# Optimization experiments

Hardware: AMD Instinct MI355X
Metric: run time of the kernel (lower is better)

## Reference

```python
import jax, jax.numpy as jnp
import numpy as np

TAU = 0.2
N_CLUSTERS = 8
FOURIER_K = 8
LATENT_DIM = 64
B = 131072
N_MINUTES = 1440
TWO_PI = 2.0 * np.pi


def setup_inputs() -> dict:
    key = jax.random.key(0)
    ks = jax.random.split(key, 6)
    item_static_emb = jax.random.normal(ks[0], (B, LATENT_DIM), dtype=jnp.float32) * 0.1
    thetas = jax.random.uniform(ks[1], (B,), dtype=jnp.float32) * TWO_PI  # absolute time phase in [0, 2pi)
    cluster_prototypes = jax.random.normal(ks[2], (N_CLUSTERS, LATENT_DIM), dtype=jnp.float32) * 0.1
    fourier_a0 = jax.random.normal(ks[3], (N_CLUSTERS, LATENT_DIM), dtype=jnp.float32) * 0.1
    fourier_a = jax.random.normal(ks[4], (N_CLUSTERS, FOURIER_K, LATENT_DIM), dtype=jnp.float32) * 0.1
    fourier_b = jax.random.normal(ks[5], (N_CLUSTERS, FOURIER_K, LATENT_DIM), dtype=jnp.float32) * 0.1
    return {
        "item_static_emb": item_static_emb,
        "thetas": thetas,
        "cluster_prototypes": cluster_prototypes,
        "fourier_a0": fourier_a0,
        "fourier_a": fourier_a,
        "fourier_b": fourier_b,
    }


def reference(item_static_emb, thetas, cluster_prototypes, fourier_a0, fourier_a, fourier_b):
    # Soft cluster routing: (B, n_clusters)
    scores = jnp.matmul(item_static_emb, cluster_prototypes.T) / TAU
    P = jax.nn.softmax(scores, axis=1)

    # Time-indexed minute bucket; torch builds tables from linspace(0, 2pi, 1440)
    # so the angle for bucket m is m * 2pi/1439.
    minute_indices = jnp.clip((thetas / TWO_PI * N_MINUTES).astype(jnp.int32), 0, N_MINUTES - 1)
    k_seq = jnp.arange(1, FOURIER_K + 1, dtype=jnp.float32)  # (K,)
    angles = minute_indices.astype(jnp.float32) * (TWO_PI / (N_MINUTES - 1))  # (B,)
    k_angles = angles[:, None] * k_seq[None, :]  # (B, K)
    cos_vals = jnp.cos(k_angles)  # (B, K)
    sin_vals = jnp.sin(k_angles)  # (B, K)

    # Fourier-series evaluation per cluster: (B, n_clusters, d)
    a_term = jnp.einsum('bk,nkd->bnd', cos_vals, fourier_a)
    b_term = jnp.einsum('bk,nkd->bnd', sin_vals, fourier_b)
    F_theta = fourier_a0[None, :, :] + a_term + b_term  # (B, n_clusters, d)

    # Softmax-weighted mixture combine: (B, d)
    item_dynamic_emb = jnp.einsum('bn,bnd->bd', P, F_theta)
    return item_dynamic_emb, P
```

## Files before the change

kernel.cpp:

```cpp
#include <hip/hip_runtime.h>
#include <hip/hip_fp16.h>
#include <math.h>

#define D 64
#define NC 8
#define FK 8
#define NMIN 1440
#define TWO_PI_F 6.28318530717958647692f

#define TSZ ((size_t)NMIN * NC * D)

__global__ __launch_bounds__(256) void build_table_kernel(
    const float* __restrict__ a0,
    const float* __restrict__ fa,
    const float* __restrict__ fb,
    __half* __restrict__ T)
{
    const int m = blockIdx.x;
    const int t = threadIdx.x;
    const int d  = t & (D - 1);
    const int n0 = t >> 6;
    const float angle = (float)m * (TWO_PI_F / (float)(NMIN - 1));

    float c[FK], s[FK];
    float s1, c1;
    sincosf(angle, &s1, &c1);
    c[0] = c1; s[0] = s1;
    {
        const float tw = 2.0f * c1;
        float cp = 1.0f, sp = 0.0f;
        float cc = c1, ss = s1;
#pragma unroll
        for (int k = 1; k < FK; ++k) {
            const float cn = fmaf(tw, cc, -cp);
            const float sn = fmaf(tw, ss, -sp);
            cp = cc; sp = ss; cc = cn; ss = sn;
            c[k] = cc; s[k] = ss;
        }
    }

#pragma unroll
    for (int j = 0; j < 2; ++j) {
        const int n = n0 + 4 * j;
        float v = a0[n * D + d];
#pragma unroll
        for (int k = 0; k < FK; ++k) {
            v = fmaf(c[k], fa[(n * FK + k) * D + d], v);
            v = fmaf(s[k], fb[(n * FK + k) * D + d], v);
        }
        T[(size_t)(m * NC + n) * D + d] = __float2half(v);
    }
}

__device__ __forceinline__ float grp8_allreduce_sum(float v) {
    int t;
    t = __builtin_amdgcn_update_dpp(0, __float_as_int(v), 0xB1, 0xF, 0xF, true);
    v += __int_as_float(t);
    t = __builtin_amdgcn_update_dpp(0, __float_as_int(v), 0x4E, 0xF, 0xF, true);
    v += __int_as_float(t);
    t = __builtin_amdgcn_update_dpp(0, __float_as_int(v), 0x141, 0xF, 0xF, true);
    v += __int_as_float(t);
    return v;
}

__global__ __launch_bounds__(256) void mix_kernel8(
    const float* __restrict__ emb,
    const float* __restrict__ thetas,
    const float* __restrict__ proto,
    const __half* __restrict__ T,
    float* __restrict__ out_emb,
    float* __restrict__ out_P,
    int B)
{
    __shared__ float4 sproto[NC * (D / 4)];
    if (threadIdx.x < NC * (D / 4)) {
        sproto[threadIdx.x] = ((const float4*)proto)[threadIdx.x];
    }
    __syncthreads();

    const int t = blockIdx.x * 256 + threadIdx.x;
    const int b = t >> 3;
    const int j = t & 7;
    if (b >= B) return;

    const float th = thetas[b];
    int m = (int)((th / TWO_PI_F) * (float)NMIN);
    m = m < 0 ? 0 : (m > NMIN - 1 ? NMIN - 1 : m);

    const float4* __restrict__ e4 = (const float4*)emb + (size_t)b * (D / 4);
    const float4 ev0 = e4[j];
    const float4 ev1 = e4[j + 8];

    const uint2* __restrict__ t2 = (const uint2*)(T + (size_t)m * NC * D);
    uint2 ua[NC], ub[NC];
#pragma unroll
    for (int n = 0; n < NC; ++n) {
        ua[n] = t2[n * 16 + j];
        ub[n] = t2[n * 16 + j + 8];
    }

    float sc[NC];
#pragma unroll
    for (int n = 0; n < NC; ++n) {
        const float4 pa = sproto[n * (D / 4) + j];
        const float4 pb = sproto[n * (D / 4) + j + 8];
        float v = ev0.x * pa.x;
        v = fmaf(ev0.y, pa.y, v);
        v = fmaf(ev0.z, pa.z, v);
        v = fmaf(ev0.w, pa.w, v);
        v = fmaf(ev1.x, pb.x, v);
        v = fmaf(ev1.y, pb.y, v);
        v = fmaf(ev1.z, pb.z, v);
        v = fmaf(ev1.w, pb.w, v);
        sc[n] = v;
    }

#pragma unroll
    for (int n = 0; n < NC; ++n) {
        sc[n] = grp8_allreduce_sum(sc[n]);
    }

    float mx = -1e30f;
#pragma unroll
    for (int n = 0; n < NC; ++n) { sc[n] *= 5.0f; mx = fmaxf(mx, sc[n]); }
    float sum = 0.0f;
#pragma unroll
    for (int n = 0; n < NC; ++n) { sc[n] = __expf(sc[n] - mx); sum += sc[n]; }
    const float inv = 1.0f / sum;
#pragma unroll
    for (int n = 0; n < NC; ++n) sc[n] *= inv;

    float4 acc0 = make_float4(0.f, 0.f, 0.f, 0.f);
    float4 acc1 = make_float4(0.f, 0.f, 0.f, 0.f);
#pragma unroll
    for (int n = 0; n < NC; ++n) {
        const float pw = sc[n];
        const float2 a01 = __half22float2(*(const __half2*)&ua[n].x);
        const float2 a23 = __half22float2(*(const __half2*)&ua[n].y);
        const float2 b01 = __half22float2(*(const __half2*)&ub[n].x);
        const float2 b23 = __half22float2(*(const __half2*)&ub[n].y);
        acc0.x = fmaf(pw, a01.x, acc0.x);
        acc0.y = fmaf(pw, a01.y, acc0.y);
        acc0.z = fmaf(pw, a23.x, acc0.z);
        acc0.w = fmaf(pw, a23.y, acc0.w);
        acc1.x = fmaf(pw, b01.x, acc1.x);
        acc1.y = fmaf(pw, b01.y, acc1.y);
        acc1.z = fmaf(pw, b23.x, acc1.z);
        acc1.w = fmaf(pw, b23.y, acc1.w);
    }

    float4* __restrict__ o4 = (float4*)out_emb + (size_t)b * (D / 4);
    o4[j]     = acc0;
    o4[j + 8] = acc1;

    if (j == 0) {
        ((float4*)out_P)[(size_t)b * 2 + 0] = make_float4(sc[0], sc[1], sc[2], sc[3]);
    } else if (j == 4) {
        ((float4*)out_P)[(size_t)b * 2 + 1] = make_float4(sc[4], sc[5], sc[6], sc[7]);
    }
}

__global__ __launch_bounds__(256) void fused_fallback(
    const float* __restrict__ emb,
    const float* __restrict__ thetas,
    const float* __restrict__ proto,
    const float* __restrict__ a0,
    const float* __restrict__ fa,
    const float* __restrict__ fb,
    float* __restrict__ out_emb,
    float* __restrict__ out_P,
    int B)
{
    __shared__ float sp[NC * D];
    __shared__ float sa0[NC * D];
    __shared__ float sfa[NC * FK * D];
    __shared__ float sfb[NC * FK * D];
    for (int i = threadIdx.x; i < NC * D; i += 256) { sp[i] = proto[i]; sa0[i] = a0[i]; }
    for (int i = threadIdx.x; i < NC * FK * D; i += 256) { sfa[i] = fa[i]; sfb[i] = fb[i]; }
    __syncthreads();

    const int b = blockIdx.x * 256 + threadIdx.x;
    if (b >= B) return;

    const float4* __restrict__ e4  = (const float4*)(emb + (size_t)b * D);
    const float4* sp4  = (const float4*)sp;
    const float4* sa04 = (const float4*)sa0;
    const float4* sfa4 = (const float4*)sfa;
    const float4* sfb4 = (const float4*)sfb;

    float sc[NC];
#pragma unroll
    for (int n = 0; n < NC; ++n) sc[n] = 0.0f;
#pragma unroll
    for (int i = 0; i < D / 4; ++i) {
        const float4 ev = e4[i];
#pragma unroll
        for (int n = 0; n < NC; ++n) {
            const float4 pv = sp4[n * (D / 4) + i];
            sc[n] = fmaf(ev.x, pv.x, sc[n]);
            sc[n] = fmaf(ev.y, pv.y, sc[n]);
            sc[n] = fmaf(ev.z, pv.z, sc[n]);
            sc[n] = fmaf(ev.w, pv.w, sc[n]);
        }
    }
    float mx = -1e30f;
#pragma unroll
    for (int n = 0; n < NC; ++n) { sc[n] *= 5.0f; mx = fmaxf(mx, sc[n]); }
    float sum = 0.0f;
#pragma unroll
    for (int n = 0; n < NC; ++n) { sc[n] = __expf(sc[n] - mx); sum += sc[n]; }
    const float inv = 1.0f / sum;
#pragma unroll
    for (int n = 0; n < NC; ++n) sc[n] *= inv;

    const float th = thetas[b];
    int m = (int)((th / TWO_PI_F) * (float)NMIN);
    m = m < 0 ? 0 : (m > NMIN - 1 ? NMIN - 1 : m);
    const float angle = (float)m * (TWO_PI_F / (float)(NMIN - 1));
    float c[FK], s[FK];
#pragma unroll
    for (int k = 0; k < FK; ++k) sincosf(angle * (float)(k + 1), &s[k], &c[k]);

    float4 acc[D / 4];
#pragma unroll
    for (int i = 0; i < D / 4; ++i) acc[i] = make_float4(0.f, 0.f, 0.f, 0.f);
#pragma unroll
    for (int n = 0; n < NC; ++n) {
        const float pw = sc[n];
#pragma unroll
        for (int i = 0; i < D / 4; ++i) {
            float4 v = sa04[n * (D / 4) + i];
#pragma unroll
            for (int k = 0; k < FK; ++k) {
                const float4 av = sfa4[(n * FK + k) * (D / 4) + i];
                const float4 bv = sfb4[(n * FK + k) * (D / 4) + i];
                v.x = fmaf(c[k], av.x, v.x); v.x = fmaf(s[k], bv.x, v.x);
                v.y = fmaf(c[k], av.y, v.y); v.y = fmaf(s[k], bv.y, v.y);
                v.z = fmaf(c[k], av.z, v.z); v.z = fmaf(s[k], bv.z, v.z);
                v.w = fmaf(c[k], av.w, v.w); v.w = fmaf(s[k], bv.w, v.w);
            }
            acc[i].x = fmaf(pw, v.x, acc[i].x);
            acc[i].y = fmaf(pw, v.y, acc[i].y);
            acc[i].z = fmaf(pw, v.z, acc[i].z);
            acc[i].w = fmaf(pw, v.w, acc[i].w);
        }
    }
    float4* o4 = (float4*)(out_emb + (size_t)b * D);
#pragma unroll
    for (int i = 0; i < D / 4; ++i) o4[i] = acc[i];
    float4* op = (float4*)(out_P + (size_t)b * NC);
    op[0] = make_float4(sc[0], sc[1], sc[2], sc[3]);
    op[1] = make_float4(sc[4], sc[5], sc[6], sc[7]);
}

extern "C" void kernel_launch(void* const* d_in, const int* in_sizes, int n_in,
                              void* d_out, int out_size, void* d_ws, size_t ws_size,
                              hipStream_t stream)
{
    const float* emb    = (const float*)d_in[0];
    const float* thetas = (const float*)d_in[1];
    const float* proto  = (const float*)d_in[2];
    const float* a0     = (const float*)d_in[3];
    const float* fa     = (const float*)d_in[4];
    const float* fb     = (const float*)d_in[5];

    const int B = in_sizes[0] / D;
    float* out_emb = (float*)d_out;
    float* out_P   = (float*)d_out + (size_t)B * D;

    const size_t table_bytes = TSZ * sizeof(__half);

    if (ws_size >= table_bytes) {
        __half* T = (__half*)d_ws;
        build_table_kernel<<<NMIN, 256, 0, stream>>>(a0, fa, fb, T);
        const long long total_threads = (long long)B * 8;
        const int blocks = (int)((total_threads + 255) / 256);
        mix_kernel8<<<blocks, 256, 0, stream>>>(emb, thetas, proto, T, out_emb, out_P, B);
    } else {
        const int blocks = (B + 255) / 256;
        fused_fallback<<<blocks, 256, 0, stream>>>(emb, thetas, proto, a0, fa, fb,
                                                   out_emb, out_P, B);
    }
}
```

Measured before the change: 26.97 us.

## Process four rows per thread group with software-prefetched next-row loads

```diff
diff --git a/kernel.cpp b/kernel.cpp
--- a/kernel.cpp
+++ b/kernel.cpp
@@ -6,6 +6,7 @@
 #define NC 8
 #define FK 8
 #define NMIN 1440
+#define ITER 4
 #define TWO_PI_F 6.28318530717958647692f
 
 #define TSZ ((size_t)NMIN * NC * D)
@@ -63,14 +64,15 @@
     return v;
 }
 
-__global__ __launch_bounds__(256) void mix_kernel8(
+__global__ __launch_bounds__(256) void mix_kernel8p(
     const float* __restrict__ emb,
     const float* __restrict__ thetas,
     const float* __restrict__ proto,
     const __half* __restrict__ T,
     float* __restrict__ out_emb,
     float* __restrict__ out_P,
-    int B)
+    int B,
+    int gstride)
 {
     __shared__ float4 sproto[NC * (D / 4)];
     if (threadIdx.x < NC * (D / 4)) {
@@ -78,85 +80,107 @@
     }
     __syncthreads();
 
-    const int t = blockIdx.x * 256 + threadIdx.x;
-    const int b = t >> 3;
-    const int j = t & 7;
-    if (b >= B) return;
-
-    const float th = thetas[b];
-    int m = (int)((th / TWO_PI_F) * (float)NMIN);
-    m = m < 0 ? 0 : (m > NMIN - 1 ? NMIN - 1 : m);
-
+    const int ggid = (blockIdx.x * 256 + threadIdx.x) >> 3;
+    const int j    = threadIdx.x & 7;
+    if (ggid >= gstride) return;
+
+    int b = ggid;
+
+    float th = thetas[b];
     const float4* __restrict__ e4 = (const float4*)emb + (size_t)b * (D / 4);
-    const float4 ev0 = e4[j];
-    const float4 ev1 = e4[j + 8];
-
-    const uint2* __restrict__ t2 = (const uint2*)(T + (size_t)m * NC * D);
-    uint2 ua[NC], ub[NC];
-#pragma unroll
-    for (int n = 0; n < NC; ++n) {
-        ua[n] = t2[n * 16 + j];
-        ub[n] = t2[n * 16 + j + 8];
-    }
-
-    float sc[NC];
-#pragma unroll
-    for (int n = 0; n < NC; ++n) {
-        const float4 pa = sproto[n * (D / 4) + j];
-        const float4 pb = sproto[n * (D / 4) + j + 8];
-        float v = ev0.x * pa.x;
-        v = fmaf(ev0.y, pa.y, v);
-        v = fmaf(ev0.z, pa.z, v);
-        v = fmaf(ev0.w, pa.w, v);
-        v = fmaf(ev1.x, pb.x, v);
-        v = fmaf(ev1.y, pb.y, v);
-        v = fmaf(ev1.z, pb.z, v);
-        v = fmaf(ev1.w, pb.w, v);
-        sc[n] = v;
-    }
-
-#pragma unroll
-    for (int n = 0; n < NC; ++n) {
-        sc[n] = grp8_allreduce_sum(sc[n]);
-    }
-
-    float mx = -1e30f;
-#pragma unroll
-    for (int n = 0; n < NC; ++n) { sc[n] *= 5.0f; mx = fmaxf(mx, sc[n]); }
-    float sum = 0.0f;
-#pragma unroll
-    for (int n = 0; n < NC; ++n) { sc[n] = __expf(sc[n] - mx); sum += sc[n]; }
-    const float inv = 1.0f / sum;
-#pragma unroll
-    for (int n = 0; n < NC; ++n) sc[n] *= inv;
-
-    float4 acc0 = make_float4(0.f, 0.f, 0.f, 0.f);
-    float4 acc1 = make_float4(0.f, 0.f, 0.f, 0.f);
-#pragma unroll
-    for (int n = 0; n < NC; ++n) {
-        const float pw = sc[n];
-        const float2 a01 = __half22float2(*(const __half2*)&ua[n].x);
-        const float2 a23 = __half22float2(*(const __half2*)&ua[n].y);
-        const float2 b01 = __half22float2(*(const __half2*)&ub[n].x);
-        const float2 b23 = __half22float2(*(const __half2*)&ub[n].y);
-        acc0.x = fmaf(pw, a01.x, acc0.x);
-        acc0.y = fmaf(pw, a01.y, acc0.y);
-        acc0.z = fmaf(pw, a23.x, acc0.z);
-        acc0.w = fmaf(pw, a23.y, acc0.w);
-        acc1.x = fmaf(pw, b01.x, acc1.x);
-        acc1.y = fmaf(pw, b01.y, acc1.y);
-        acc1.z = fmaf(pw, b23.x, acc1.z);
-        acc1.w = fmaf(pw, b23.y, acc1.w);
-    }
-
-    float4* __restrict__ o4 = (float4*)out_emb + (size_t)b * (D / 4);
-    o4[j]     = acc0;
-    o4[j + 8] = acc1;
-
-    if (j == 0) {
-        ((float4*)out_P)[(size_t)b * 2 + 0] = make_float4(sc[0], sc[1], sc[2], sc[3]);
-    } else if (j == 4) {
-        ((float4*)out_P)[(size_t)b * 2 + 1] = make_float4(sc[4], sc[5], sc[6], sc[7]);
+    float4 ev0 = e4[j];
+    float4 ev1 = e4[j + 8];
+
+#pragma unroll
+    for (int i = 0; i < ITER; ++i) {
+        if (b < B) {
+            const int bn = b + gstride;
+            const bool have_next = (i + 1 < ITER) && (bn < B);
+            float th_n = 0.0f;
+            float4 en0, en1;
+            if (have_next) {
+                th_n = thetas[bn];
+                const float4* __restrict__ e4n = (const float4*)emb + (size_t)bn * (D / 4);
+                en0 = e4n[j];
+                en1 = e4n[j + 8];
+            }
+
+            int m = (int)((th / TWO_PI_F) * (float)NMIN);
+            m = m < 0 ? 0 : (m > NMIN - 1 ? NMIN - 1 : m);
+
+            const uint2* __restrict__ t2 = (const uint2*)(T + (size_t)m * NC * D);
+            uint2 ua[NC], ub[NC];
+#pragma unroll
+            for (int n = 0; n < NC; ++n) {
+                ua[n] = t2[n * 16 + j];
+                ub[n] = t2[n * 16 + j + 8];
+            }
+
+            float sc[NC];
+#pragma unroll
+            for (int n = 0; n < NC; ++n) {
+                const float4 pa = sproto[n * (D / 4) + j];
+                const float4 pb = sproto[n * (D / 4) + j + 8];
+                float v = ev0.x * pa.x;
+                v = fmaf(ev0.y, pa.y, v);
+                v = fmaf(ev0.z, pa.z, v);
+                v = fmaf(ev0.w, pa.w, v);
+                v = fmaf(ev1.x, pb.x, v);
+                v = fmaf(ev1.y, pb.y, v);
+                v = fmaf(ev1.z, pb.z, v);
+                v = fmaf(ev1.w, pb.w, v);
+                sc[n] = v;
+            }
+
+#pragma unroll
+            for (int n = 0; n < NC; ++n) {
+                sc[n] = grp8_allreduce_sum(sc[n]);
+            }
+
+            float mx = -1e30f;
+#pragma unroll
+            for (int n = 0; n < NC; ++n) { sc[n] *= 5.0f; mx = fmaxf(mx, sc[n]); }
+            float sum = 0.0f;
+#pragma unroll
+            for (int n = 0; n < NC; ++n) { sc[n] = __expf(sc[n] - mx); sum += sc[n]; }
+            const float inv = 1.0f / sum;
+#pragma unroll
+            for (int n = 0; n < NC; ++n) sc[n] *= inv;
+
+            float4 acc0 = make_float4(0.f, 0.f, 0.f, 0.f);
+            float4 acc1 = make_float4(0.f, 0.f, 0.f, 0.f);
+#pragma unroll
+            for (int n = 0; n < NC; ++n) {
+                const float pw = sc[n];
+                const float2 a01 = __half22float2(*(const __half2*)&ua[n].x);
+                const float2 a23 = __half22float2(*(const __half2*)&ua[n].y);
+                const float2 b01 = __half22float2(*(const __half2*)&ub[n].x);
+                const float2 b23 = __half22float2(*(const __half2*)&ub[n].y);
+                acc0.x = fmaf(pw, a01.x, acc0.x);
+                acc0.y = fmaf(pw, a01.y, acc0.y);
+                acc0.z = fmaf(pw, a23.x, acc0.z);
+                acc0.w = fmaf(pw, a23.y, acc0.w);
+                acc1.x = fmaf(pw, b01.x, acc1.x);
+                acc1.y = fmaf(pw, b01.y, acc1.y);
+                acc1.z = fmaf(pw, b23.x, acc1.z);
+                acc1.w = fmaf(pw, b23.y, acc1.w);
+            }
+
+            float4* __restrict__ o4 = (float4*)out_emb + (size_t)b * (D / 4);
+            o4[j]     = acc0;
+            o4[j + 8] = acc1;
+
+            if (j == 0) {
+                ((float4*)out_P)[(size_t)b * 2 + 0] = make_float4(sc[0], sc[1], sc[2], sc[3]);
+            } else if (j == 4) {
+                ((float4*)out_P)[(size_t)b * 2 + 1] = make_float4(sc[4], sc[5], sc[6], sc[7]);
+            }
+
+            b  = bn;
+            th = th_n;
+            ev0 = en0;
+            ev1 = en1;
+        }
     }
 }
 
@@ -273,9 +297,11 @@
     if (ws_size >= table_bytes) {
         __half* T = (__half*)d_ws;
         build_table_kernel<<<NMIN, 256, 0, stream>>>(a0, fa, fb, T);
-        const long long total_threads = (long long)B * 8;
+        const int gstride = (B + ITER - 1) / ITER;
+        const long long total_threads = (long long)gstride * 8;
         const int blocks = (int)((total_threads + 255) / 256);
-        mix_kernel8<<<blocks, 256, 0, stream>>>(emb, thetas, proto, T, out_emb, out_P, B);
+        mix_kernel8p<<<blocks, 256, 0, stream>>>(emb, thetas, proto, T,
+                                                 out_emb, out_P, B, gstride);
     } else {
         const int blocks = (B + 255) / 256;
         fused_fallback<<<blocks, 256, 0, stream>>>(emb, thetas, proto, a0, fa, fb,
```

Measured after the change: 27.69 us. 1.03x slower.
